# Optimization experiments

Measured on AMD Instinct MI355X. Metric: run time of the kernel, lower is better.

The kernel has to match this reference:

```python
import jax, jax.numpy as jnp
import numpy as np

V, E, H, S, B = 32000, 512, 512, 512, 32  # vocab, emb=n_unit, hidden, srclen, batch


def _lstm_zero_state_step(x, W_ih, b_ih, b_hh):
    """PyTorch LSTM single step with zero initial (h, c).
    With h0 = 0, the recurrent term h0 @ W_hh^T vanishes, so W_hh does not
    affect the output (faithful to the original, which never passes state).
    Gate order i, f, g, o. Works on [..., in_dim] batched inputs.
    """
    gates = x @ W_ih.T + b_ih + b_hh
    i, f, g, o = jnp.split(gates, 4, axis=-1)
    c = jax.nn.sigmoid(i) * jnp.tanh(g)  # f gate multiplies c0 = 0
    h = jax.nn.sigmoid(o) * jnp.tanh(c)
    return h, c


def setup_inputs() -> dict:
    key = jax.random.key(0)
    ks = jax.random.split(key, 10)
    s = 1.0 / np.sqrt(H)
    return {
        "src_seqs": jax.random.randint(ks[0], (S, B), 0, V),
        "W_emb": jax.random.normal(ks[1], (V, E), dtype=jnp.float32) * 0.02,
        # read LSTM (E -> H)
        "W_ih_r": jax.random.uniform(ks[2], (4 * H, E), minval=-s, maxval=s),
        "b_ih_r": jax.random.uniform(ks[3], (4 * H,), minval=-s, maxval=s),
        "b_hh_r": jax.random.uniform(ks[4], (4 * H,), minval=-s, maxval=s),
        # compose MLP (2H -> 2H)
        "W_c": jax.random.uniform(ks[5], (2 * H, 2 * H), minval=-s, maxval=s),
        "b_c": jax.random.uniform(ks[6], (2 * H,), minval=-s, maxval=s),
        # write LSTM (2H -> H)
        "W_ih_w": jax.random.uniform(ks[7], (4 * H, 2 * H), minval=-s, maxval=s),
        "b_ih_w": jax.random.uniform(ks[8], (4 * H,), minval=-s, maxval=s),
        "b_hh_w": jax.random.uniform(ks[9], (4 * H,), minval=-s, maxval=s),
    }


def reference(src_seqs, W_emb, W_ih_r, b_ih_r, b_hh_r, W_c, b_c,
              W_ih_w, b_ih_w, b_hh_w):
    emb = W_emb[src_seqs]                     # [S, B, E]
    # read LSTM is stateless per step (zero init state each call) -> vectorize
    o_all, _ = _lstm_zero_state_step(emb, W_ih_r, b_ih_r, b_hh_r)  # [S, B, H]
    M0 = jnp.transpose(emb, (1, 0, 2))        # [B, S, H] memory

    def step(M, o_t):
        # read: attention over memory
        z = jax.nn.softmax(jnp.einsum('bsh,bh->bs', M, o_t), axis=1)  # [B, S]
        m = jnp.einsum('bs,bsh->bh', z, M)                            # [B, H]
        # compose
        c_in = jnp.concatenate([o_t, m], axis=1) @ W_c.T + b_c        # [B, 2H]
        # write LSTM (also stateless per call)
        h, cell = _lstm_zero_state_step(c_in, W_ih_w, b_ih_w, b_hh_w)  # [B, H]
        # erase/write memory update
        M_new = (1.0 - z)[..., None] * M + z[..., None] * h[:, None, :]
        return M_new, (h, cell)

    _, (hs, cells) = jax.lax.scan(step, M0, o_all)
    outputs = hs                              # [S, B, H]
    h_n = hs[-1][None]                        # [1, B, H] (n_layer=1)
    c_n = cells[-1][None]                     # [1, B, H]
    return outputs, h_n, c_n
```

## Files before the change

kernel.cpp:

```cpp
#include <hip/hip_runtime.h>
#include <hip/hip_bf16.h>

#define S_LEN 512
#define B_SZ  32
#define H_DIM 512
#define KC    1024

typedef __attribute__((ext_vector_type(8)))  short  short8;
typedef __attribute__((ext_vector_type(4)))  float  f32x4;
typedef __attribute__((ext_vector_type(2)))  float  f32x2;

static __device__ __forceinline__ unsigned short f2bf(float f){
  unsigned u = __float_as_uint(f);
  u += 0x7fffu + ((u >> 16) & 1u);
  return (unsigned short)(u >> 16);
}
static __device__ __forceinline__ short8 cvt8(float4 a, float4 b){
  short8 r;
  r[0]=(short)f2bf(a.x); r[1]=(short)f2bf(a.y); r[2]=(short)f2bf(a.z); r[3]=(short)f2bf(a.w);
  r[4]=(short)f2bf(b.x); r[5]=(short)f2bf(b.y); r[6]=(short)f2bf(b.z); r[7]=(short)f2bf(b.w);
  return r;
}
static __device__ __forceinline__ float sigf(float x){ return 1.0f/(1.0f+__expf(-x)); }
static __device__ __forceinline__ float tanh_(float x){
  float e = __expf(2.0f*x);
  return (e-1.0f)/(e+1.0f);
}

__global__ __launch_bounds__(256) void k_gather_emb(const int* __restrict__ src,
    const float* __restrict__ Wemb, unsigned short* __restrict__ embB){
  int gid = blockIdx.x*256 + threadIdx.x;
  int row = gid >> 6;
  int k   = (gid & 63) * 8;
  int idx = src[row];
  const float* p = Wemb + (size_t)idx*H_DIM + k;
  float4 a = *(const float4*)p;
  float4 b = *(const float4*)(p+4);
  *(short8*)(embB + (size_t)gid*8) = cvt8(a,b);
}

__global__ __launch_bounds__(256) void k_perm_wr(const float* __restrict__ W,
    unsigned short* __restrict__ out){
  int gid = blockIdx.x*256 + threadIdx.x;
  int n = gid >> 6;
  int k = (gid & 63)*8;
  int j = (n&3)*512 + (n>>2);
  const float* p = W + (size_t)j*512 + k;
  float4 a = *(const float4*)p;
  float4 b = *(const float4*)(p+4);
  *(short8*)(out + (size_t)gid*8) = cvt8(a,b);
}

__global__ __launch_bounds__(256) void k_perm_wihw(const float* __restrict__ W,
    unsigned short* __restrict__ out){
  int gid = blockIdx.x*256 + threadIdx.x;
  int n = gid >> 7;
  int k = (gid & 127)*8;
  int j = (n&3)*512 + (n>>2);
  const float* p = W + (size_t)j*KC + k;
  float4 a = *(const float4*)p;
  float4 b = *(const float4*)(p+4);
  *(short8*)(out + (size_t)gid*8) = cvt8(a,b);
}

__global__ __launch_bounds__(256) void k_wcT(const float* __restrict__ Wc,
    unsigned short* __restrict__ out){
  __shared__ float tile[64][65];
  int bx = blockIdx.x & 15, by = blockIdx.x >> 4;
  int c0 = bx*64, r0 = by*64;
  int row = threadIdx.x >> 2;
  int cp  = (threadIdx.x & 3)*16;
  for (int i=0;i<16;i+=4){
    float4 v = *(const float4*)&Wc[(size_t)(r0+row)*KC + c0 + cp + i];
    tile[row][cp+i+0]=v.x; tile[row][cp+i+1]=v.y; tile[row][cp+i+2]=v.z; tile[row][cp+i+3]=v.w;
  }
  __syncthreads();
  short8 s0, s1;
  for(int i=0;i<8;++i){
    s0[i]=(short)f2bf(tile[cp+i][row]);
    s1[i]=(short)f2bf(tile[cp+8+i][row]);
  }
  unsigned short* op = out + (size_t)(c0+row)*KC + r0 + cp;
  *(short8*)op = s0; *(short8*)(op+8) = s1;
}

__global__ __launch_bounds__(256) void k_bias_r(const float* __restrict__ bi,
    const float* __restrict__ bh, float* __restrict__ out){
  int n = blockIdx.x*256 + threadIdx.x;
  int j = (n&3)*512 + (n>>2);
  out[n] = bi[j] + bh[j];
}

__global__ __launch_bounds__(256) void k_bcomb(const float* __restrict__ Wihw,
    const float* __restrict__ bc, const float* __restrict__ bi,
    const float* __restrict__ bh, float* __restrict__ out){
  int n = blockIdx.x*256 + threadIdx.x;
  int j = (n&3)*512 + (n>>2);
  const float* wp = Wihw + (size_t)j*KC;
  float s = 0.f;
  for (int l=0;l<KC;l+=4){
    float4 w = *(const float4*)&wp[l];
    float4 c = *(const float4*)&bc[l];
    s += w.x*c.x + w.y*c.y + w.z*c.z + w.w*c.w;
  }
  out[n] = s + bi[j] + bh[j];
}

template<int EPI>
__global__ __launch_bounds__(256) void gemm_k(const unsigned short* __restrict__ A,
    const unsigned short* __restrict__ Bm, int K, int bStride, int bnCnt,
    const float* __restrict__ bias, float* __restrict__ outF,
    unsigned short* __restrict__ outB, short* __restrict__ outI, int outStride){
  __shared__ __align__(16) char smem[66560];
  unsigned short* As = (unsigned short*)smem;
  unsigned short* Bs = As + 128*72;
  float* epi = (float*)smem;
  const int tid = threadIdx.x, lane = tid & 63, w = tid >> 6;
  const int wr = w >> 1, wc = w & 1;
  const int bm = blockIdx.x / bnCnt, bn = blockIdx.x % bnCnt;
  f32x4 acc[4][4] = {};
  const size_t Abase = (size_t)bm*128*K;
  const size_t Bbase = (size_t)bn*128*bStride;
  for (int k0 = 0; k0 < K; k0 += 64){
    __syncthreads();
    #pragma unroll
    for (int i = 0; i < 4; ++i){
      int idx = tid + i*256;
      int row = idx >> 3, cb = (idx & 7)*8;
      *(short8*)&As[row*72 + cb] = *(const short8*)&A[Abase + (size_t)row*K + k0 + cb];
      *(short8*)&Bs[row*72 + cb] = *(const short8*)&Bm[Bbase + (size_t)row*bStride + k0 + cb];
    }
    __syncthreads();
    #pragma unroll
    for (int kk = 0; kk < 64; kk += 32){
      short8 af[4], bf[4];
      #pragma unroll
      for (int i=0;i<4;++i) af[i] = *(short8*)&As[(wr*64 + i*16 + (lane&15))*72 + kk + (lane>>4)*8];
      #pragma unroll
      for (int j=0;j<4;++j) bf[j] = *(short8*)&Bs[(wc*64 + j*16 + (lane&15))*72 + kk + (lane>>4)*8];
      #pragma unroll
      for (int i=0;i<4;++i)
        #pragma unroll
        for (int j=0;j<4;++j)
          acc[i][j] = __builtin_amdgcn_mfma_f32_16x16x32_bf16(af[i], bf[j], acc[i][j], 0,0,0);
    }
  }
  if (EPI == 0){
    float bj[4];
    #pragma unroll
    for (int j=0;j<4;++j) bj[j] = bias[bn*128 + wc*64 + j*16 + (lane&15)];
    __syncthreads();
    float* ep = epi + w*(64*65);
    #pragma unroll
    for (int i=0;i<4;++i)
      #pragma unroll
      for (int j=0;j<4;++j)
        #pragma unroll
        for (int r=0;r<4;++r)
          ep[(i*16 + (lane>>4)*4 + r)*65 + j*16 + (lane&15)] = acc[i][j][r] + bj[j];
    __syncthreads();
    int rg = bm*128 + wr*64 + lane;
    #pragma unroll
    for (int q=0;q<16;++q){
      float gi = ep[lane*65 + q*4+0];
      float gg = ep[lane*65 + q*4+2];
      float go = ep[lane*65 + q*4+3];
      float c = sigf(gi)*tanh_(gg);
      float h = sigf(go)*tanh_(c);
      int cg = bn*32 + wc*16 + q;
      outF[(size_t)rg*H_DIM + cg] = h;
      outB[(size_t)rg*H_DIM + cg] = f2bf(h);
    }
  } else if (EPI == 1){
    #pragma unroll
    for (int i=0;i<4;++i)
      #pragma unroll
      for (int j=0;j<4;++j)
        #pragma unroll
        for (int r=0;r<4;++r){
          int rg = bm*128 + wr*64 + i*16 + (lane>>4)*4 + r;
          int cg = bn*128 + wc*64 + j*16 + (lane&15);
          outB[(size_t)rg*outStride + cg] = f2bf(acc[i][j][r]);
        }
  } else {
    #pragma unroll
    for (int i=0;i<4;++i)
      #pragma unroll
      for (int j=0;j<4;++j)
        #pragma unroll
        for (int r=0;r<4;++r){
          int rg = bm*128 + wr*64 + i*16 + (lane>>4)*4 + r;
          int cg = bn*128 + wc*64 + j*16 + (lane&15);
          float v = acc[i][j][r] * 4096.0f;
          v = fminf(fmaxf(v, -32767.0f), 32767.0f);
          outI[(size_t)rg*outStride + cg] = (short)__float2int_rn(v);
        }
  }
}

__global__ __launch_bounds__(256,1) void scan_k(
    const int* __restrict__ src, const float* __restrict__ Wemb,
    const float* __restrict__ o_all, const unsigned short* __restrict__ Wcomb,
    const float* __restrict__ bcomb, const short* __restrict__ gatesO,
    float* __restrict__ dpart, float* __restrict__ mpart,
    float* __restrict__ out, int* __restrict__ cnts){
  __shared__ __align__(16) float M[512*66];
  __shared__ __align__(16) float dstage[512];
  __shared__ __align__(16) float m_full[512];
  __shared__ __align__(16) float z_lds[512];
  __shared__ float part4[256];
  __shared__ float gsum[256];
  __shared__ float m_sl[64];
  __shared__ float o_sl[64];
  __shared__ float h_lds[64];
  __shared__ float red4[4];

  const int tid = threadIdx.x, lane = tid & 63, wv = tid >> 6;
  const int bid = blockIdx.x;
  const int c = bid & 7, b = bid >> 3;
  const int r15 = lane & 15, kq = lane >> 4;
  int* dcnt = cnts + b*64;
  int* mcnt = cnts + 2048 + b*64;
  float* dslot = dpart + ((size_t)b*8 + c)*512;
  float* mslot = mpart + (size_t)b*512 + c*64;

  short8 wf[64];
  #pragma unroll
  for (int ct=0; ct<4; ++ct)
    #pragma unroll
    for (int kf=0; kf<16; ++kf)
      wf[ct*16+kf] = *(const short8*)&Wcomb[
        (size_t)(c*256 + wv*64 + ct*16 + r15)*KC + 512 + kf*32 + kq*8];

  z_lds[tid] = 0.f; z_lds[tid+256] = 0.f;
  if (tid < 64){
    h_lds[tid] = 0.f;
    o_sl[tid] = o_all[(size_t)b*H_DIM + c*64 + tid];
  }
  __syncthreads();
  #pragma unroll
  for (int r=0;r<2;++r){
    int s = tid + r*256;
    int idx = src[s*B_SZ + b];
    const float* wp = Wemb + (size_t)idx*H_DIM + c*64;
    float* mp = &M[s*66];
    float dd = 0.f;
    #pragma unroll
    for (int k=0;k<64;k+=4){
      float4 v = *(const float4*)&wp[k];
      *(f32x2*)&mp[k]   = (f32x2){v.x, v.y};
      *(f32x2*)&mp[k+2] = (f32x2){v.z, v.w};
      dd += v.x*o_sl[k] + v.y*o_sl[k+1] + v.z*o_sl[k+2] + v.w*o_sl[k+3];
    }
    dstage[s] = dd;
  }
  __syncthreads();
  {
    f32x2 v = *(f32x2*)&dstage[2*tid];
    float* p = dslot + 2*tid;
    asm volatile("global_store_dwordx2 %0, %1, off sc0 sc1" :: "v"(p), "v"(v) : "memory");
  }
  asm volatile("s_waitcnt vmcnt(0)" ::: "memory");
  __syncthreads();
  if (tid == 0)
    __hip_atomic_fetch_add(dcnt, 1, __ATOMIC_RELAXED, __HIP_MEMORY_SCOPE_AGENT);

  for (int t=0; t<S_LEN; ++t){
    const int tn = (t < S_LEN-1) ? t+1 : t;
    float opf = 0.f;
    if (tid < 64) opf = o_all[((size_t)tn*B_SZ + b)*H_DIM + c*64 + tid];
    float gO = (float)gatesO[((size_t)t*B_SZ + b)*2048 + c*256 + tid] * (1.0f/4096.0f);

    if (tid == 0){
      int tg = 8*(t+1);
      while (__hip_atomic_load(dcnt, __ATOMIC_RELAXED, __HIP_MEMORY_SCOPE_AGENT) < tg)
        __builtin_amdgcn_s_sleep(1);
    }
    __syncthreads();
    asm volatile("" ::: "memory");

    float d0, d1;
    {
      const float* p0 = dpart + (size_t)b*8*512 + 2*tid;
      f32x2 a0,a1,a2,a3,a4,a5,a6,a7;
      asm volatile(
        "global_load_dwordx2 %0, %8, off sc0 sc1\n\t"
        "global_load_dwordx2 %1, %9, off sc0 sc1\n\t"
        "global_load_dwordx2 %2, %10, off sc0 sc1\n\t"
        "global_load_dwordx2 %3, %11, off sc0 sc1\n\t"
        "global_load_dwordx2 %4, %12, off sc0 sc1\n\t"
        "global_load_dwordx2 %5, %13, off sc0 sc1\n\t"
        "global_load_dwordx2 %6, %14, off sc0 sc1\n\t"
        "global_load_dwordx2 %7, %15, off sc0 sc1\n\t"
        "s_waitcnt vmcnt(0)"
        : "=&v"(a0),"=&v"(a1),"=&v"(a2),"=&v"(a3),
          "=&v"(a4),"=&v"(a5),"=&v"(a6),"=&v"(a7)
        : "v"(p0), "v"(p0+512), "v"(p0+1024), "v"(p0+1536),
          "v"(p0+2048), "v"(p0+2560), "v"(p0+3072), "v"(p0+3584)
        : "memory");
      d0 = ((a0[0]+a1[0])+(a2[0]+a3[0])) + ((a4[0]+a5[0])+(a6[0]+a7[0]));
      d1 = ((a0[1]+a1[1])+(a2[1]+a3[1])) + ((a4[1]+a5[1])+(a6[1]+a7[1]));
    }
    float mx, sm;
    {
      float v = fmaxf(d0, d1);
      #pragma unroll
      for (int m2=32;m2>0;m2>>=1) v = fmaxf(v, __shfl_xor(v, m2));
      __syncthreads();
      if (lane==0) red4[wv] = v;
      __syncthreads();
      mx = fmaxf(fmaxf(red4[0],red4[1]), fmaxf(red4[2],red4[3]));
    }
    float ex0 = __expf(d0 - mx), ex1 = __expf(d1 - mx);
    {
      float v = ex0 + ex1;
      #pragma unroll
      for (int m2=32;m2>0;m2>>=1) v += __shfl_xor(v, m2);
      __syncthreads();
      if (lane==0) red4[wv] = v;
      __syncthreads();
      sm = (red4[0]+red4[1]) + (red4[2]+red4[3]);
    }
    float inv = 1.f / sm;
    z_lds[2*tid]   = ex0*inv;
    z_lds[2*tid+1] = ex1*inv;
    __syncthreads();

    {
      int col = tid & 63;
      int s0 = wv*128;
      float mp = 0.f;
      #pragma unroll 8
      for (int s2=0;s2<128;++s2)
        mp += z_lds[s0+s2]*M[(s0+s2)*66 + col];
      part4[wv*64 + col] = mp;
    }
    __syncthreads();
    if (tid < 64)
      m_sl[tid] = (part4[tid]+part4[64+tid]) + (part4[128+tid]+part4[192+tid]);
    __syncthreads();
    if (tid < 16){
      f32x4 v = *(f32x4*)&m_sl[tid*4];
      float* p = mslot + tid*4;
      asm volatile("global_store_dwordx4 %0, %1, off sc0 sc1" :: "v"(p), "v"(v) : "memory");
    }
    asm volatile("s_waitcnt vmcnt(0)" ::: "memory");
    __syncthreads();
    if (tid == 0){
      __hip_atomic_fetch_add(mcnt, 1, __ATOMIC_RELAXED, __HIP_MEMORY_SCOPE_AGENT);
      int tg = 8*(t+1);
      while (__hip_atomic_load(mcnt, __ATOMIC_RELAXED, __HIP_MEMORY_SCOPE_AGENT) < tg)
        __builtin_amdgcn_s_sleep(1);
    }
    __syncthreads();
    asm volatile("" ::: "memory");

    {
      const float* p = mpart + (size_t)b*512 + 2*tid;
      f32x2 v;
      asm volatile(
        "global_load_dwordx2 %0, %1, off sc0 sc1\n\t"
        "s_waitcnt vmcnt(0)" : "=&v"(v) : "v"(p) : "memory");
      m_full[2*tid] = v[0]; m_full[2*tid+1] = v[1];
    }
    __syncthreads();

    {
      short8 a[16];
      #pragma unroll
      for (int kf=0; kf<16; ++kf){
        short8 v = {0,0,0,0,0,0,0,0};
        if (r15 == 0){
          int kb = kf*32 + kq*8;
          #pragma unroll
          for (int j=0;j<8;++j) v[j] = (short)f2bf(m_full[kb+j]);
        }
        a[kf] = v;
      }
      f32x4 acc0 = {0,0,0,0}, acc1 = acc0, acc2 = acc0, acc3 = acc0;
      #pragma unroll
      for (int kf=0; kf<16; ++kf){
        acc0 = __builtin_amdgcn_mfma_f32_16x16x32_bf16(a[kf], wf[kf],    acc0, 0,0,0);
        acc1 = __builtin_amdgcn_mfma_f32_16x16x32_bf16(a[kf], wf[16+kf], acc1, 0,0,0);
        acc2 = __builtin_amdgcn_mfma_f32_16x16x32_bf16(a[kf], wf[32+kf], acc2, 0,0,0);
        acc3 = __builtin_amdgcn_mfma_f32_16x16x32_bf16(a[kf], wf[48+kf], acc3, 0,0,0);
      }
      if (lane < 16){
        gsum[wv*64 + lane]      = acc0[0];
        gsum[wv*64 + 16 + lane] = acc1[0];
        gsum[wv*64 + 32 + lane] = acc2[0];
        gsum[wv*64 + 48 + lane] = acc3[0];
      }
    }
    __syncthreads();

    {
      float gv = gsum[tid] + gO + bcomb[c*256 + tid];
      __syncthreads();
      part4[tid] = gv;
    }
    __syncthreads();
    if (tid < 64){
      float gi = part4[tid*4+0];
      float gG = part4[tid*4+2];
      float go = part4[tid*4+3];
      float ccv = sigf(gi)*tanh_(gG);
      float hh  = sigf(go)*tanh_(ccv);
      h_lds[tid] = hh;
      int hq = c*64 + tid;
      out[((size_t)t*B_SZ + b)*H_DIM + hq] = hh;
      if (t == S_LEN-1){
        out[(size_t)S_LEN*B_SZ*H_DIM + (size_t)b*H_DIM + hq] = hh;
        out[(size_t)S_LEN*B_SZ*H_DIM + (size_t)B_SZ*H_DIM + (size_t)b*H_DIM + hq] = ccv;
      }
      o_sl[tid] = opf;
    }
    __syncthreads();

    if (t < S_LEN-1){
      #pragma unroll
      for (int r=0;r<2;++r){
        int s = tid + r*256;
        float zp = z_lds[s];
        float* mp = &M[s*66];
        float dd = 0.f;
        #pragma unroll
        for (int k=0;k<64;k+=2){
          f32x2 v = *(f32x2*)&mp[k];
          f32x2 h2 = *(f32x2*)&h_lds[k];
          f32x2 o2 = *(f32x2*)&o_sl[k];
          v[0] += zp*(h2[0]-v[0]); v[1] += zp*(h2[1]-v[1]);
          *(f32x2*)&mp[k] = v;
          dd += v[0]*o2[0] + v[1]*o2[1];
        }
        dstage[s] = dd;
      }
      __syncthreads();
      {
        f32x2 v = *(f32x2*)&dstage[2*tid];
        float* p = dslot + 2*tid;
        asm volatile("global_store_dwordx2 %0, %1, off sc0 sc1" :: "v"(p), "v"(v) : "memory");
      }
      asm volatile("s_waitcnt vmcnt(0)" ::: "memory");
      __syncthreads();
      if (tid == 0)
        __hip_atomic_fetch_add(dcnt, 1, __ATOMIC_RELAXED, __HIP_MEMORY_SCOPE_AGENT);
    }
  }
}

extern "C" void kernel_launch(void* const* d_in, const int* in_sizes, int n_in,
                              void* d_out, int out_size, void* d_ws, size_t ws_size,
                              hipStream_t stream){
  const int*   src   = (const int*)  d_in[0];
  const float* Wemb  = (const float*)d_in[1];
  const float* Wihr  = (const float*)d_in[2];
  const float* bihr  = (const float*)d_in[3];
  const float* bhhr  = (const float*)d_in[4];
  const float* Wc    = (const float*)d_in[5];
  const float* bc    = (const float*)d_in[6];
  const float* Wihw  = (const float*)d_in[7];
  const float* bihw  = (const float*)d_in[8];
  const float* bhhw  = (const float*)d_in[9];
  float* out = (float*)d_out;

  char* ws = (char*)d_ws;
  size_t off = 0;
  auto alloc = [&](size_t bytes)->char*{
    char* p = ws + off; off += (bytes + 255) & ~(size_t)255; return p;
  };
  unsigned short* embB  = (unsigned short*)alloc((size_t)16384*512*2);
  float*          o_all = (float*)         alloc((size_t)16384*512*4);
  unsigned short* o_allB= (unsigned short*)alloc((size_t)16384*512*2);
  unsigned short* WrP   = (unsigned short*)alloc((size_t)2048*512*2);
  unsigned short* WiwP  = (unsigned short*)alloc((size_t)2048*1024*2);
  unsigned short* WcT   = (unsigned short*)alloc((size_t)1024*1024*2);
  unsigned short* Wcomb = (unsigned short*)alloc((size_t)2048*1024*2);
  float*          bperm = (float*)alloc(2048*4);
  float*          bcomb = (float*)alloc(2048*4);
  short*          gatesO= (short*)alloc((size_t)16384*2048*2);
  float*          dpart = (float*)alloc((size_t)32*8*512*4);
  float*          mpart = (float*)alloc((size_t)32*512*4);
  int*            cnts  = (int*)  alloc(16384);

  hipMemsetAsync(cnts, 0, 16384, stream);
  k_gather_emb<<<4096,256,0,stream>>>(src, Wemb, embB);
  k_perm_wr  <<<512, 256,0,stream>>>(Wihr, WrP);
  k_perm_wihw<<<1024,256,0,stream>>>(Wihw, WiwP);
  k_wcT      <<<256, 256,0,stream>>>(Wc, WcT);
  k_bias_r   <<<8,   256,0,stream>>>(bihr, bhhr, bperm);
  k_bcomb    <<<8,   256,0,stream>>>(Wihw, bc, bihw, bhhw, bcomb);
  gemm_k<0><<<2048,256,0,stream>>>(embB, WrP, 512, 512, 16, bperm, o_all, o_allB, nullptr, H_DIM);
  gemm_k<1><<<128,256,0,stream>>>(WiwP, WcT, 1024, 1024, 8, nullptr, nullptr, Wcomb, nullptr, 1024);
  gemm_k<2><<<2048,256,0,stream>>>(o_allB, Wcomb, 512, 1024, 16, nullptr, nullptr, nullptr, gatesO, 2048);
  scan_k<<<256,256,0,stream>>>(src, Wemb, o_all, Wcomb, bcomb, gatesO,
                               dpart, mpart, out, cnts);
}
```

Before: 6.410 ms.

## Defer memory update to next step and merge cross-block barriers via algebraic score update

Restructures the per-step scan so the erase/write update of M and its partial dot products run one step late, overlapped with the attention read. The score for step t is rebuilt algebraically from the previous step's pre-update dot products plus a small h·o scalar published per block with a step-tagged flag. This merges the two global counter barriers per step into one and publishes the score partials together with the m partials. The cost is an extra polled handshake on the hslot flags, more LDS, and some floating-point reassociation in the scores.

```diff
diff --git a/kernel.cpp b/kernel.cpp
--- a/kernel.cpp
+++ b/kernel.cpp
@@ -203,26 +203,29 @@
     const float* __restrict__ o_all, const unsigned short* __restrict__ Wcomb,
     const float* __restrict__ bcomb, const short* __restrict__ gatesO,
     float* __restrict__ dpart, float* __restrict__ mpart,
-    float* __restrict__ out, int* __restrict__ cnts){
+    float* __restrict__ hslot, float* __restrict__ out, int* __restrict__ cnts){
   __shared__ __align__(16) float M[512*66];
+  __shared__ __align__(16) float z2[2][512];
+  __shared__ __align__(16) float dd0s[512];
   __shared__ __align__(16) float dstage[512];
   __shared__ __align__(16) float m_full[512];
-  __shared__ __align__(16) float z_lds[512];
   __shared__ float part4[256];
   __shared__ float gsum[256];
+  __shared__ float gg[256];
   __shared__ float m_sl[64];
   __shared__ float o_sl[64];
   __shared__ float h_lds[64];
   __shared__ float red4[4];
+  __shared__ float hdot_sh;
 
   const int tid = threadIdx.x, lane = tid & 63, wv = tid >> 6;
   const int bid = blockIdx.x;
   const int c = bid & 7, b = bid >> 3;
   const int r15 = lane & 15, kq = lane >> 4;
-  int* dcnt = cnts + b*64;
-  int* mcnt = cnts + 2048 + b*64;
+  int* cnt1 = cnts + b*64;
   float* dslot = dpart + ((size_t)b*8 + c)*512;
   float* mslot = mpart + (size_t)b*512 + c*64;
+  float* myhs  = hslot + ((size_t)b*8 + c)*2;
 
   short8 wf[64];
   #pragma unroll
@@ -232,7 +235,7 @@
       wf[ct*16+kf] = *(const short8*)&Wcomb[
         (size_t)(c*256 + wv*64 + ct*16 + r15)*KC + 512 + kf*32 + kq*8];
 
-  z_lds[tid] = 0.f; z_lds[tid+256] = 0.f;
+  z2[1][tid] = 0.f; z2[1][tid+256] = 0.f;
   if (tid < 64){
     h_lds[tid] = 0.f;
     o_sl[tid] = o_all[(size_t)b*H_DIM + c*64 + tid];
@@ -262,45 +265,75 @@
   }
   asm volatile("s_waitcnt vmcnt(0)" ::: "memory");
   __syncthreads();
-  if (tid == 0)
-    __hip_atomic_fetch_add(dcnt, 1, __ATOMIC_RELAXED, __HIP_MEMORY_SCOPE_AGENT);
+  if (tid == 0){
+    __hip_atomic_fetch_add(cnt1, 1, __ATOMIC_RELAXED, __HIP_MEMORY_SCOPE_AGENT);
+    while (__hip_atomic_load(cnt1, __ATOMIC_RELAXED, __HIP_MEMORY_SCOPE_AGENT) < 8)
+      __builtin_amdgcn_s_sleep(1);
+  }
+  __syncthreads();
+  asm volatile("" ::: "memory");
+  {
+    const float* p0 = dpart + (size_t)b*8*512 + 2*tid;
+    f32x2 a0,a1,a2,a3,a4,a5,a6,a7;
+    asm volatile(
+      "global_load_dwordx2 %0, %8, off sc0 sc1\n\t"
+      "global_load_dwordx2 %1, %9, off sc0 sc1\n\t"
+      "global_load_dwordx2 %2, %10, off sc0 sc1\n\t"
+      "global_load_dwordx2 %3, %11, off sc0 sc1\n\t"
+      "global_load_dwordx2 %4, %12, off sc0 sc1\n\t"
+      "global_load_dwordx2 %5, %13, off sc0 sc1\n\t"
+      "global_load_dwordx2 %6, %14, off sc0 sc1\n\t"
+      "global_load_dwordx2 %7, %15, off sc0 sc1\n\t"
+      "s_waitcnt vmcnt(0)"
+      : "=&v"(a0),"=&v"(a1),"=&v"(a2),"=&v"(a3),
+        "=&v"(a4),"=&v"(a5),"=&v"(a6),"=&v"(a7)
+      : "v"(p0), "v"(p0+512), "v"(p0+1024), "v"(p0+1536),
+        "v"(p0+2048), "v"(p0+2560), "v"(p0+3072), "v"(p0+3584)
+      : "memory");
+    dd0s[2*tid]   = ((a0[0]+a1[0])+(a2[0]+a3[0])) + ((a4[0]+a5[0])+(a6[0]+a7[0]));
+    dd0s[2*tid+1] = ((a0[1]+a1[1])+(a2[1]+a3[1])) + ((a4[1]+a5[1])+(a6[1]+a7[1]));
+  }
+  __syncthreads();
 
   for (int t=0; t<S_LEN; ++t){
+    const int cur = t & 1, pv = cur ^ 1;
     const int tn = (t < S_LEN-1) ? t+1 : t;
     float opf = 0.f;
     if (tid < 64) opf = o_all[((size_t)tn*B_SZ + b)*H_DIM + c*64 + tid];
     float gO = (float)gatesO[((size_t)t*B_SZ + b)*2048 + c*256 + tid] * (1.0f/4096.0f);
 
-    if (tid == 0){
-      int tg = 8*(t+1);
-      while (__hip_atomic_load(dcnt, __ATOMIC_RELAXED, __HIP_MEMORY_SCOPE_AGENT) < tg)
-        __builtin_amdgcn_s_sleep(1);
-    }
-    __syncthreads();
-    asm volatile("" ::: "memory");
-
-    float d0, d1;
-    {
-      const float* p0 = dpart + (size_t)b*8*512 + 2*tid;
-      f32x2 a0,a1,a2,a3,a4,a5,a6,a7;
-      asm volatile(
-        "global_load_dwordx2 %0, %8, off sc0 sc1\n\t"
-        "global_load_dwordx2 %1, %9, off sc0 sc1\n\t"
-        "global_load_dwordx2 %2, %10, off sc0 sc1\n\t"
-        "global_load_dwordx2 %3, %11, off sc0 sc1\n\t"
-        "global_load_dwordx2 %4, %12, off sc0 sc1\n\t"
-        "global_load_dwordx2 %5, %13, off sc0 sc1\n\t"
-        "global_load_dwordx2 %6, %14, off sc0 sc1\n\t"
-        "global_load_dwordx2 %7, %15, off sc0 sc1\n\t"
-        "s_waitcnt vmcnt(0)"
-        : "=&v"(a0),"=&v"(a1),"=&v"(a2),"=&v"(a3),
-          "=&v"(a4),"=&v"(a5),"=&v"(a6),"=&v"(a7)
-        : "v"(p0), "v"(p0+512), "v"(p0+1024), "v"(p0+1536),
-          "v"(p0+2048), "v"(p0+2560), "v"(p0+3072), "v"(p0+3584)
-        : "memory");
-      d0 = ((a0[0]+a1[0])+(a2[0]+a3[0])) + ((a4[0]+a5[0])+(a6[0]+a7[0]));
-      d1 = ((a0[1]+a1[1])+(a2[1]+a3[1])) + ((a4[1]+a5[1])+(a6[1]+a7[1]));
-    }
+    float hdot = 0.f;
+    if (t > 0){
+      if (wv == 0){
+        bool mine = (lane < 8);
+        const float* p = hslot + ((size_t)b*8 + (lane & 7))*2;
+        float myval = 0.f;
+        for(;;){
+          bool ok = true;
+          if (mine){
+            f32x2 hv;
+            asm volatile("global_load_dwordx2 %0, %1, off sc0 sc1\n\ts_waitcnt vmcnt(0)"
+                         : "=&v"(hv) : "v"(p) : "memory");
+            myval = hv[0];
+            ok = (__float_as_int(hv[1]) == t-1);
+          }
+          if (__all(ok)) break;
+          __builtin_amdgcn_s_sleep(1);
+        }
+        float v = mine ? myval : 0.f;
+        v += __shfl_xor(v,1); v += __shfl_xor(v,2); v += __shfl_xor(v,4);
+        if (lane == 0) hdot_sh = v;
+      }
+      __syncthreads();
+      hdot = hdot_sh;
+    } else {
+      __syncthreads();
+    }
+    if (tid < 64) o_sl[tid] = opf;
+
+    float zp0 = z2[pv][2*tid], zp1 = z2[pv][2*tid+1];
+    float d0 = (1.f - zp0)*dd0s[2*tid]   + zp0*hdot;
+    float d1 = (1.f - zp1)*dd0s[2*tid+1] + zp1*hdot;
     float mx, sm;
     {
       float v = fmaxf(d0, d1);
@@ -322,8 +355,26 @@
       sm = (red4[0]+red4[1]) + (red4[2]+red4[3]);
     }
     float inv = 1.f / sm;
-    z_lds[2*tid]   = ex0*inv;
-    z_lds[2*tid+1] = ex1*inv;
+    z2[cur][2*tid]   = ex0*inv;
+    z2[cur][2*tid+1] = ex1*inv;
+
+    #pragma unroll
+    for (int r=0;r<2;++r){
+      int s = tid + r*256;
+      float zp = z2[pv][s];
+      float* mp = &M[s*66];
+      float dd = 0.f;
+      #pragma unroll
+      for (int k=0;k<64;k+=2){
+        f32x2 v = *(f32x2*)&mp[k];
+        f32x2 h2 = *(f32x2*)&h_lds[k];
+        f32x2 o2 = *(f32x2*)&o_sl[k];
+        v[0] += zp*(h2[0]-v[0]); v[1] += zp*(h2[1]-v[1]);
+        *(f32x2*)&mp[k] = v;
+        dd += v[0]*o2[0] + v[1]*o2[1];
+      }
+      dstage[s] = dd;
+    }
     __syncthreads();
 
     {
@@ -332,36 +383,58 @@
       float mp = 0.f;
       #pragma unroll 8
       for (int s2=0;s2<128;++s2)
-        mp += z_lds[s0+s2]*M[(s0+s2)*66 + col];
+        mp += z2[cur][s0+s2]*M[(s0+s2)*66 + col];
       part4[wv*64 + col] = mp;
     }
     __syncthreads();
     if (tid < 64)
       m_sl[tid] = (part4[tid]+part4[64+tid]) + (part4[128+tid]+part4[192+tid]);
     __syncthreads();
-    if (tid < 16){
-      f32x4 v = *(f32x4*)&m_sl[tid*4];
-      float* p = mslot + tid*4;
-      asm volatile("global_store_dwordx4 %0, %1, off sc0 sc1" :: "v"(p), "v"(v) : "memory");
+
+    {
+      f32x2 v = *(f32x2*)&dstage[2*tid];
+      float* p = dslot + 2*tid;
+      asm volatile("global_store_dwordx2 %0, %1, off sc0 sc1" :: "v"(p), "v"(v) : "memory");
+      if (tid < 16){
+        f32x4 mv = *(f32x4*)&m_sl[tid*4];
+        float* q = mslot + tid*4;
+        asm volatile("global_store_dwordx4 %0, %1, off sc0 sc1" :: "v"(q), "v"(mv) : "memory");
+      }
     }
     asm volatile("s_waitcnt vmcnt(0)" ::: "memory");
     __syncthreads();
     if (tid == 0){
-      __hip_atomic_fetch_add(mcnt, 1, __ATOMIC_RELAXED, __HIP_MEMORY_SCOPE_AGENT);
-      int tg = 8*(t+1);
-      while (__hip_atomic_load(mcnt, __ATOMIC_RELAXED, __HIP_MEMORY_SCOPE_AGENT) < tg)
+      __hip_atomic_fetch_add(cnt1, 1, __ATOMIC_RELAXED, __HIP_MEMORY_SCOPE_AGENT);
+      int tg = 8*(t+2);
+      while (__hip_atomic_load(cnt1, __ATOMIC_RELAXED, __HIP_MEMORY_SCOPE_AGENT) < tg)
         __builtin_amdgcn_s_sleep(1);
     }
     __syncthreads();
     asm volatile("" ::: "memory");
 
     {
-      const float* p = mpart + (size_t)b*512 + 2*tid;
-      f32x2 v;
+      const float* pm = mpart + (size_t)b*512 + 2*tid;
+      const float* p0 = dpart + (size_t)b*8*512 + 2*tid;
+      f32x2 mv,a0,a1,a2,a3,a4,a5,a6,a7;
       asm volatile(
-        "global_load_dwordx2 %0, %1, off sc0 sc1\n\t"
-        "s_waitcnt vmcnt(0)" : "=&v"(v) : "v"(p) : "memory");
-      m_full[2*tid] = v[0]; m_full[2*tid+1] = v[1];
+        "global_load_dwordx2 %0, %9, off sc0 sc1\n\t"
+        "global_load_dwordx2 %1, %10, off sc0 sc1\n\t"
+        "global_load_dwordx2 %2, %11, off sc0 sc1\n\t"
+        "global_load_dwordx2 %3, %12, off sc0 sc1\n\t"
+        "global_load_dwordx2 %4, %13, off sc0 sc1\n\t"
+        "global_load_dwordx2 %5, %14, off sc0 sc1\n\t"
+        "global_load_dwordx2 %6, %15, off sc0 sc1\n\t"
+        "global_load_dwordx2 %7, %16, off sc0 sc1\n\t"
+        "global_load_dwordx2 %8, %17, off sc0 sc1\n\t"
+        "s_waitcnt vmcnt(0)"
+        : "=&v"(mv),"=&v"(a0),"=&v"(a1),"=&v"(a2),"=&v"(a3),
+          "=&v"(a4),"=&v"(a5),"=&v"(a6),"=&v"(a7)
+        : "v"(pm), "v"(p0), "v"(p0+512), "v"(p0+1024), "v"(p0+1536),
+          "v"(p0+2048), "v"(p0+2560), "v"(p0+3072), "v"(p0+3584)
+        : "memory");
+      m_full[2*tid] = mv[0]; m_full[2*tid+1] = mv[1];
+      dd0s[2*tid]   = ((a0[0]+a1[0])+(a2[0]+a3[0])) + ((a4[0]+a5[0])+(a6[0]+a7[0]));
+      dd0s[2*tid+1] = ((a0[1]+a1[1])+(a2[1]+a3[1])) + ((a4[1]+a5[1])+(a6[1]+a7[1]));
     }
     __syncthreads();
 
@@ -393,17 +466,13 @@
       }
     }
     __syncthreads();
-
-    {
-      float gv = gsum[tid] + gO + bcomb[c*256 + tid];
-      __syncthreads();
-      part4[tid] = gv;
-    }
-    __syncthreads();
+    gg[tid] = gsum[tid] + gO + bcomb[c*256 + tid];
+    __syncthreads();
+
     if (tid < 64){
-      float gi = part4[tid*4+0];
-      float gG = part4[tid*4+2];
-      float go = part4[tid*4+3];
+      float gi = gg[tid*4+0];
+      float gG = gg[tid*4+2];
+      float go = gg[tid*4+3];
       float ccv = sigf(gi)*tanh_(gG);
       float hh  = sigf(go)*tanh_(ccv);
       h_lds[tid] = hh;
@@ -413,39 +482,15 @@
         out[(size_t)S_LEN*B_SZ*H_DIM + (size_t)b*H_DIM + hq] = hh;
         out[(size_t)S_LEN*B_SZ*H_DIM + (size_t)B_SZ*H_DIM + (size_t)b*H_DIM + hq] = ccv;
       }
-      o_sl[tid] = opf;
-    }
-    __syncthreads();
-
-    if (t < S_LEN-1){
-      #pragma unroll
-      for (int r=0;r<2;++r){
-        int s = tid + r*256;
-        float zp = z_lds[s];
-        float* mp = &M[s*66];
-        float dd = 0.f;
-        #pragma unroll
-        for (int k=0;k<64;k+=2){
-          f32x2 v = *(f32x2*)&mp[k];
-          f32x2 h2 = *(f32x2*)&h_lds[k];
-          f32x2 o2 = *(f32x2*)&o_sl[k];
-          v[0] += zp*(h2[0]-v[0]); v[1] += zp*(h2[1]-v[1]);
-          *(f32x2*)&mp[k] = v;
-          dd += v[0]*o2[0] + v[1]*o2[1];
-        }
-        dstage[s] = dd;
-      }
-      __syncthreads();
-      {
-        f32x2 v = *(f32x2*)&dstage[2*tid];
-        float* p = dslot + 2*tid;
-        asm volatile("global_store_dwordx2 %0, %1, off sc0 sc1" :: "v"(p), "v"(v) : "memory");
-      }
-      asm volatile("s_waitcnt vmcnt(0)" ::: "memory");
-      __syncthreads();
-      if (tid == 0)
-        __hip_atomic_fetch_add(dcnt, 1, __ATOMIC_RELAXED, __HIP_MEMORY_SCOPE_AGENT);
-    }
+      float hp = hh * o_sl[tid];
+      hp += __shfl_xor(hp,1); hp += __shfl_xor(hp,2); hp += __shfl_xor(hp,4);
+      hp += __shfl_xor(hp,8); hp += __shfl_xor(hp,16); hp += __shfl_xor(hp,32);
+      if (tid == 0){
+        f32x2 pk; pk[0] = hp; pk[1] = __int_as_float(t);
+        asm volatile("global_store_dwordx2 %0, %1, off sc0 sc1" :: "v"(myhs), "v"(pk) : "memory");
+      }
+    }
+    __syncthreads();
   }
 }
 
@@ -481,9 +526,11 @@
   short*          gatesO= (short*)alloc((size_t)16384*2048*2);
   float*          dpart = (float*)alloc((size_t)32*8*512*4);
   float*          mpart = (float*)alloc((size_t)32*512*4);
+  float*          hpart = (float*)alloc((size_t)32*8*2*4);
   int*            cnts  = (int*)  alloc(16384);
 
   hipMemsetAsync(cnts, 0, 16384, stream);
+  hipMemsetAsync(hpart, 0xFF, 2048, stream);
   k_gather_emb<<<4096,256,0,stream>>>(src, Wemb, embB);
   k_perm_wr  <<<512, 256,0,stream>>>(Wihr, WrP);
   k_perm_wihw<<<1024,256,0,stream>>>(Wihw, WiwP);
@@ -494,5 +541,5 @@
   gemm_k<1><<<128,256,0,stream>>>(WiwP, WcT, 1024, 1024, 8, nullptr, nullptr, Wcomb, nullptr, 1024);
   gemm_k<2><<<2048,256,0,stream>>>(o_allB, Wcomb, 512, 1024, 16, nullptr, nullptr, nullptr, gatesO, 2048);
   scan_k<<<256,256,0,stream>>>(src, Wemb, o_all, Wcomb, bcomb, gatesO,
-                               dpart, mpart, out, cnts);
-}
+                               dpart, mpart, hpart, out, cnts);
+}
```

Result: no change. 6.512 ms (+1.6%).
